# Performance work log

Measured on AMD Instinct MI355X. Metric: run time of the kernel, lower is better.

## Reference

```python
import jax, jax.numpy as jnp
import numpy as np

N_NODES = 100000
N_EDGES = 1600000
D_IN = 128
D_HID = 128


def setup_inputs() -> dict:
    key = jax.random.key(0)
    ks = jax.random.split(key, 7)
    s_in = 1.0 / np.sqrt(D_IN)
    s_hid = 1.0 / np.sqrt(D_HID)
    return {
        "x": jax.random.normal(ks[0], (N_NODES, D_IN), dtype=jnp.float32),
        "edge_index": jax.random.randint(ks[1], (2, N_EDGES), 0, N_NODES, dtype=jnp.int64),
        "W1_l": jax.random.normal(ks[2], (D_IN, D_HID), dtype=jnp.float32) * s_in,
        "b1": jnp.zeros((D_HID,), dtype=jnp.float32),
        "W1_r": jax.random.normal(ks[3], (D_IN, D_HID), dtype=jnp.float32) * s_in,
        "W2_l": jax.random.normal(ks[4], (D_HID, D_HID), dtype=jnp.float32) * s_hid,
        "b2": jnp.zeros((D_HID,), dtype=jnp.float32),
        "W2_r": jax.random.normal(ks[5], (D_HID, D_HID), dtype=jnp.float32) * s_hid,
    }


def _mean_aggregate(x, src, dst, num_nodes):
    # messages x[src] mean-aggregated at dst (PyG SAGEConv default aggr='mean')
    msg = jnp.take(x, src, axis=0)                       # [E, D] gather
    summed = jax.ops.segment_sum(msg, dst, num_segments=num_nodes)  # [N, D]
    deg = jax.ops.segment_sum(jnp.ones((src.shape[0],), x.dtype), dst,
                              num_segments=num_nodes)
    return summed / jnp.maximum(deg, 1.0)[:, None]


def _sage_conv(x, src, dst, W_l, b, W_r):
    agg = _mean_aggregate(x, src, dst, x.shape[0])
    # out = lin_l(aggregated neighbors) + lin_r(root)
    return agg @ W_l + b + x @ W_r


def reference(x, edge_index, W1_l, b1, W1_r, W2_l, b2, W2_r):
    src, dst = edge_index[0], edge_index[1]
    h = _sage_conv(x, src, dst, W1_l, b1, W1_r)
    h = jax.nn.relu(h)  # dropout inactive in eval mode
    out = _sage_conv(h, src, dst, W2_l, b2, W2_r)
    return out
```

## Files before the change

### kernel.cpp

```cpp
#include <hip/hip_runtime.h>

#define NN 100000
#define NE 1600000
#define DF 128
#define NBUCK 391
#define PA_BLOCKS 784
#define PB_BLOCKS 391
#define CX_BLOCKS 3125
#define CW_BLOCKS 64
#define AGG_GRID 3128

typedef short short8 __attribute__((ext_vector_type(8)));
typedef float floatx4 __attribute__((ext_vector_type(4)));
typedef float floatx2 __attribute__((ext_vector_type(2)));
typedef unsigned int uintx4 __attribute__((ext_vector_type(4)));
typedef unsigned int uint;
typedef unsigned short ushort;
typedef unsigned char uchar;

static __device__ __forceinline__ ushort f2bf(float f) {
    uint u = __builtin_bit_cast(uint, f);
    return (ushort)((u + 0x7fffu + ((u >> 16) & 1u)) >> 16);
}

__global__ __launch_bounds__(256) void pA_hist(const int* __restrict__ dst,
                                               int* __restrict__ gcnt) {
    __shared__ int h[NBUCK];
    int tid = threadIdx.x;
    for (int i = tid; i < NBUCK; i += 256) h[i] = 0;
    __syncthreads();
    int eb = blockIdx.x * 2048 + tid;
    #pragma unroll
    for (int k = 0; k < 8; ++k) {
        int e = eb + k * 256;
        if (e < NE) atomicAdd(&h[dst[e] >> 8], 1);
    }
    __syncthreads();
    for (int i = tid; i < NBUCK; i += 256)
        if (h[i]) atomicAdd(&gcnt[i], h[i]);
}

__global__ __launch_bounds__(512) void pS_scan(const int* __restrict__ gcnt,
                                               int* __restrict__ goff,
                                               int* __restrict__ gcur) {
    __shared__ int s[512];
    int tid = threadIdx.x;
    int v = (tid < NBUCK) ? gcnt[tid] : 0;
    s[tid] = v;
    __syncthreads();
    for (int st = 1; st < 512; st <<= 1) {
        int t = (tid >= st) ? s[tid - st] : 0;
        __syncthreads();
        s[tid] += t;
        __syncthreads();
    }
    if (tid < NBUCK) {
        int e = s[tid] - v;
        goff[tid] = e;
        gcur[tid] = e;
    }
    if (tid == 0) goff[NBUCK] = NE;
}

__global__ __launch_bounds__(512) void fused_mid(
        const int* __restrict__ src, const int* __restrict__ dst,
        int* __restrict__ gcur, uint2* __restrict__ pairs,
        const float* __restrict__ x, ushort* __restrict__ xb, uint* __restrict__ xf8,
        const float* __restrict__ W1l, const float* __restrict__ W1r,
        const float* __restrict__ W2l, const float* __restrict__ W2r,
        ushort* __restrict__ WT1, ushort* __restrict__ WT2) {
    __shared__ int h[NBUCK];
    __shared__ int base[NBUCK];
    int bid = blockIdx.x;
    int tid = threadIdx.x;
    if (bid < PB_BLOCKS) {
        for (int i = tid; i < NBUCK; i += 512) h[i] = 0;
        __syncthreads();
        int eb = bid * 4096 + tid;
        int bkt[8], dv[8];
        #pragma unroll
        for (int k = 0; k < 8; ++k) {
            int e = eb + k * 512;
            bkt[k] = -1;
            if (e < NE) {
                int d = dst[e];
                dv[k] = d;
                bkt[k] = d >> 8;
                atomicAdd(&h[bkt[k]], 1);
            }
        }
        __syncthreads();
        for (int i = tid; i < NBUCK; i += 512) {
            base[i] = h[i] ? atomicAdd(&gcur[i], h[i]) : 0;
            h[i] = 0;
        }
        __syncthreads();
        #pragma unroll
        for (int k = 0; k < 8; ++k) {
            int e = eb + k * 512;
            if (e < NE) {
                int r = atomicAdd(&h[bkt[k]], 1);
                pairs[base[bkt[k]] + r] = make_uint2((uint)src[e], (uint)dv[k]);
            }
        }
    } else if (bid < PB_BLOCKS + CX_BLOCKS) {
        int j = (bid - PB_BLOCKS) * 512 + tid;
        const float4* xr = (const float4*)x + (size_t)j * 2;
        float4 v0 = xr[0], v1 = xr[1];
        uint4 ob;
        ob.x = (uint)f2bf(v0.x) | ((uint)f2bf(v0.y) << 16);
        ob.y = (uint)f2bf(v0.z) | ((uint)f2bf(v0.w) << 16);
        ob.z = (uint)f2bf(v1.x) | ((uint)f2bf(v1.y) << 16);
        ob.w = (uint)f2bf(v1.z) | ((uint)f2bf(v1.w) << 16);
        ((uint4*)xb)[j] = ob;
        uint pk0 = (uint)__builtin_amdgcn_cvt_pk_fp8_f32(v0.x, v0.y, 0, false);
        pk0 = (uint)__builtin_amdgcn_cvt_pk_fp8_f32(v0.z, v0.w, (int)pk0, true);
        uint pk1 = (uint)__builtin_amdgcn_cvt_pk_fp8_f32(v1.x, v1.y, 0, false);
        pk1 = (uint)__builtin_amdgcn_cvt_pk_fp8_f32(v1.z, v1.w, (int)pk1, true);
        ((uint2*)xf8)[j] = make_uint2(pk0, pk1);
    } else {
        int id = (bid - PB_BLOCKS - CX_BLOCKS) * 512 + tid;
        int n = id >> 8, k = id & 255;
        float a = (k < 128) ? W1l[k * 128 + n] : W1r[(k - 128) * 128 + n];
        float b = (k < 128) ? W2l[k * 128 + n] : W2r[(k - 128) * 128 + n];
        WT1[id] = f2bf(a);
        WT2[id] = f2bf(b);
    }
}

__global__ __launch_bounds__(256) void pC_scatter(const uint2* __restrict__ pairs,
                                                  const int* __restrict__ goff,
                                                  int* __restrict__ off,
                                                  int* __restrict__ srt) {
    __shared__ int deg[256];
    __shared__ int loc[256];
    int b = blockIdx.x;
    int beg = goff[b], end = goff[b + 1];
    int tid = threadIdx.x;
    deg[tid] = 0;
    __syncthreads();
    for (int i = beg + tid; i < end; i += 256)
        atomicAdd(&deg[pairs[i].y & 255], 1);
    __syncthreads();
    int v = deg[tid];
    loc[tid] = v;
    __syncthreads();
    for (int st = 1; st < 256; st <<= 1) {
        int t = (tid >= st) ? loc[tid - st] : 0;
        __syncthreads();
        loc[tid] += t;
        __syncthreads();
    }
    int excl = loc[tid] - v + beg;
    int n = (b << 8) + tid;
    if (n < NN) off[n] = excl;
    __syncthreads();
    deg[tid] = excl;
    __syncthreads();
    for (int i = beg + tid; i < end; i += 256) {
        uint2 pr = pairs[i];
        int pos = atomicAdd(&deg[pr.y & 255], 1);
        srt[pos] = (int)pr.x;
    }
}

static __device__ __forceinline__ void acc16(floatx2* ac, uint4 v) {
    ac[0] += __builtin_amdgcn_cvt_pk_f32_fp8((int)v.x, false);
    ac[1] += __builtin_amdgcn_cvt_pk_f32_fp8((int)v.x, true);
    ac[2] += __builtin_amdgcn_cvt_pk_f32_fp8((int)v.y, false);
    ac[3] += __builtin_amdgcn_cvt_pk_f32_fp8((int)v.y, true);
    ac[4] += __builtin_amdgcn_cvt_pk_f32_fp8((int)v.z, false);
    ac[5] += __builtin_amdgcn_cvt_pk_f32_fp8((int)v.z, true);
    ac[6] += __builtin_amdgcn_cvt_pk_f32_fp8((int)v.w, false);
    ac[7] += __builtin_amdgcn_cvt_pk_f32_fp8((int)v.w, true);
}

#define AGG_LOOP(IDX)                                            \
    {                                                            \
        int i = lb;                                              \
        for (; i + 8 <= le; i += 8) {                            \
            int idx[8];                                          \
            _Pragma("unroll")                                    \
            for (int k = 0; k < 8; ++k) idx[k] = IDX(i + k);     \
            uint4 v[8];                                          \
            _Pragma("unroll")                                    \
            for (int k = 0; k < 8; ++k) v[k] = f[(size_t)idx[k] * 8]; \
            _Pragma("unroll")                                    \
            for (int k = 0; k < 8; ++k) acc16(ac, v[k]);         \
        }                                                        \
        if (i + 4 <= le) {                                       \
            int idx[4];                                          \
            _Pragma("unroll")                                    \
            for (int k = 0; k < 4; ++k) idx[k] = IDX(i + k);     \
            uint4 v[4];                                          \
            _Pragma("unroll")                                    \
            for (int k = 0; k < 4; ++k) v[k] = f[(size_t)idx[k] * 8]; \
            _Pragma("unroll")                                    \
            for (int k = 0; k < 4; ++k) acc16(ac, v[k]);         \
            i += 4;                                              \
        }                                                        \
        for (; i < le; ++i) {                                    \
            uint4 v = f[(size_t)IDX(i) * 8];                     \
            acc16(ac, v);                                        \
        }                                                        \
    }

__global__ __launch_bounds__(256) void agg_csr(const uint* __restrict__ feat8,
                                               const int* __restrict__ srt,
                                               const int* __restrict__ off,
                                               ushort* __restrict__ aggb) {
    __shared__ int sidx[2048];
    int nb = blockIdx.x * 32;
    if (nb >= NN) return;
    int tid = threadIdx.x;

    int segb = off[nb];
    int nend = nb + 32;
    int sege = (nend < NN) ? off[nend] : NE;
    int stage = min(sege - segb, 2048);
    for (int i = tid; i < stage; i += 256) sidx[i] = srt[segb + i];
    __syncthreads();

    int n = nb + (tid >> 3);
    int l = tid & 7;
    if (n >= NN) return;
    const uint4* f = (const uint4*)feat8 + l;

    int beg = off[n];
    int end = (n < NN - 1) ? off[n + 1] : NE;
    int lb = beg - segb, le = end - segb;

    floatx2 ac[8];
    #pragma unroll
    for (int t = 0; t < 8; ++t) ac[t] = (floatx2){0.f, 0.f};

    if (le <= stage) {
        #define IDX_LDS(ii) sidx[ii]
        AGG_LOOP(IDX_LDS)
        #undef IDX_LDS
    } else {
        #define IDX_GBL(ii) srt[segb + (ii)]
        AGG_LOOP(IDX_GBL)
        #undef IDX_GBL
    }

    float inv = 1.0f / fmaxf((float)(end - beg), 1.0f);
    uintx4 o0, o1;
    o0.x = (uint)f2bf(ac[0].x * inv) | ((uint)f2bf(ac[0].y * inv) << 16);
    o0.y = (uint)f2bf(ac[1].x * inv) | ((uint)f2bf(ac[1].y * inv) << 16);
    o0.z = (uint)f2bf(ac[2].x * inv) | ((uint)f2bf(ac[2].y * inv) << 16);
    o0.w = (uint)f2bf(ac[3].x * inv) | ((uint)f2bf(ac[3].y * inv) << 16);
    o1.x = (uint)f2bf(ac[4].x * inv) | ((uint)f2bf(ac[4].y * inv) << 16);
    o1.y = (uint)f2bf(ac[5].x * inv) | ((uint)f2bf(ac[5].y * inv) << 16);
    o1.z = (uint)f2bf(ac[6].x * inv) | ((uint)f2bf(ac[6].y * inv) << 16);
    o1.w = (uint)f2bf(ac[7].x * inv) | ((uint)f2bf(ac[7].y * inv) << 16);
    uintx4* dp = (uintx4*)(aggb + (size_t)n * 128 + l * 16);
    __builtin_nontemporal_store(o0, dp);
    __builtin_nontemporal_store(o1, dp + 1);
}

template <int RELU, int BF16OUT, int F8OUT>
__global__ __launch_bounds__(512, 4) void gemm_mfma(
        const ushort* __restrict__ aggb, const ushort* __restrict__ selfb,
        const ushort* __restrict__ WT, const float* __restrict__ bias,
        void* __restrict__ outv, uchar* __restrict__ f8out) {
    __shared__ ushort sWT[128 * 256];
    const int tid = threadIdx.x;
    const int blk = blockIdx.x;

    #pragma unroll
    for (int it = 0; it < 8; ++it) {
        int flat = it * 512 + tid;
        int col = flat >> 5;
        int c = flat & 31;
        uint4 v = *(const uint4*)(WT + (size_t)col * 256 + c * 8);
        *(uint4*)&sWT[col * 256 + (c ^ (col & 7)) * 8] = v;
    }

    const int w = tid >> 6;
    const int lane = tid & 63;
    const int m = lane & 15;
    const int q = lane >> 4;

    int node_m = blk * 128 + w * 16 + m;
    int cn = node_m < NN ? node_m : NN - 1;
    const ushort* arow = aggb + (size_t)cn * 128;
    const ushort* xrow = selfb + (size_t)cn * 128;
    short8 a[8];
    #pragma unroll
    for (int kk = 0; kk < 4; ++kk) {
        a[kk]     = *(const short8*)(arow + kk * 32 + q * 8);
        a[4 + kk] = *(const short8*)(xrow + kk * 32 + q * 8);
    }

    __syncthreads();

    floatx4 acc[8];
    #pragma unroll
    for (int t = 0; t < 8; ++t) acc[t] = (floatx4){0.f, 0.f, 0.f, 0.f};

    const int m7 = m & 7;
    #pragma unroll
    for (int kk = 0; kk < 8; ++kk) {
        int cx = (kk * 4 + q) ^ m7;
        #pragma unroll
        for (int t = 0; t < 8; ++t) {
            short8 b = *(const short8*)&sWT[(t * 16 + m) * 256 + cx * 8];
            acc[t] = __builtin_amdgcn_mfma_f32_16x16x32_bf16(a[kk], b, acc[t], 0, 0, 0);
        }
    }

    const int node_base = blk * 128 + w * 16 + q * 4;
    #pragma unroll
    for (int t = 0; t < 8; ++t) {
        int col = t * 16 + m;
        float bj = bias[col];
        #pragma unroll
        for (int r = 0; r < 4; ++r) {
            int node = node_base + r;
            if (node < NN) {
                float v = acc[t][r] + bj;
                if (RELU) v = fmaxf(v, 0.0f);
                if (BF16OUT)
                    ((ushort*)outv)[(size_t)node * 128 + col] = f2bf(v);
                else
                    ((float*)outv)[(size_t)node * 128 + col] = v;
                if (F8OUT) {
                    uint pk = (uint)__builtin_amdgcn_cvt_pk_fp8_f32(v, v, 0, false);
                    f8out[(size_t)node * 128 + col] = (uchar)pk;
                }
            }
        }
    }
}

extern "C" void kernel_launch(void* const* d_in, const int* in_sizes, int n_in,
                              void* d_out, int out_size, void* d_ws, size_t ws_size,
                              hipStream_t stream) {
    const float* x   = (const float*)d_in[0];
    const int*   ei  = (const int*)d_in[1];
    const float* W1l = (const float*)d_in[2];
    const float* b1  = (const float*)d_in[3];
    const float* W1r = (const float*)d_in[4];
    const float* W2l = (const float*)d_in[5];
    const float* b2  = (const float*)d_in[6];
    const float* W2r = (const float*)d_in[7];
    float*       out = (float*)d_out;

    const int* src = ei;
    const int* dst = ei + NE;

    char* ws = (char*)d_ws;
    int*    off  = (int*)(ws);
    int*    srt  = (int*)(ws + 400000);
    ushort* WT1  = (ushort*)(ws + 7200000);
    ushort* WT2  = (ushort*)(ws + 7265536);
    ushort* xb   = (ushort*)(ws + 7331072);
    uint*   xf8  = (uint*)(ws + 32931072);
    ushort* aggb = (ushort*)(ws + 45731072);
    ushort* hb   = (ushort*)(ws + 71331072);
    uchar*  hf8  = (uchar*)xf8;
    uint2*  pairs = (uint2*)aggb;
    int*    gcnt  = (int*)((char*)aggb + 12800000);
    int*    goff  = (int*)((char*)aggb + 12801600);
    int*    gcur  = (int*)((char*)aggb + 12803200);

    (void)hipMemsetAsync(gcnt, 0, NBUCK * 4, stream);
    pA_hist<<<PA_BLOCKS, 256, 0, stream>>>(dst, gcnt);
    pS_scan<<<1, 512, 0, stream>>>(gcnt, goff, gcur);
    fused_mid<<<PB_BLOCKS + CX_BLOCKS + CW_BLOCKS, 512, 0, stream>>>(
        src, dst, gcur, pairs, x, xb, xf8, W1l, W1r, W2l, W2r, WT1, WT2);
    pC_scatter<<<NBUCK, 256, 0, stream>>>(pairs, goff, off, srt);

    const int gemm_grid = (NN + 127) / 128;

    agg_csr<<<AGG_GRID, 256, 0, stream>>>(xf8, srt, off, aggb);
    gemm_mfma<1, 1, 1><<<gemm_grid, 512, 0, stream>>>(aggb, xb, WT1, b1, hb, hf8);

    agg_csr<<<AGG_GRID, 256, 0, stream>>>((const uint*)hf8, srt, off, aggb);
    gemm_mfma<0, 0, 0><<<gemm_grid, 512, 0, stream>>>(aggb, hb, WT2, b2, out, nullptr);
}
```

Before: 195.2 us.

## Replace atomic bucket partitioning with per-block histogram, column scan, and stored ranks

The histogram pass now records each edge's local rank within its block bucket and writes per-block histograms instead of atomically accumulating global counts. A new column-scan kernel computes per-block exclusive offsets for each bucket, so the partition pass can compute each edge's destination deterministically without shared-memory atomics or global atomicAdd on cursors. This removes the memset, the duplicated histogram and atomics in fused_mid, at the cost of an extra kernel launch and extra traffic for the 3.2MB rank array and 1.2MB histogram table.

```diff
diff --git a/kernel.cpp b/kernel.cpp
--- a/kernel.cpp
+++ b/kernel.cpp
@@ -24,7 +24,8 @@
 }
 
 __global__ __launch_bounds__(256) void pA_hist(const int* __restrict__ dst,
-                                               int* __restrict__ gcnt) {
+                                               int* __restrict__ hist,
+                                               ushort* __restrict__ rank8) {
     __shared__ int h[NBUCK];
     int tid = threadIdx.x;
     for (int i = tid; i < NBUCK; i += 256) h[i] = 0;
@@ -33,19 +34,52 @@
     #pragma unroll
     for (int k = 0; k < 8; ++k) {
         int e = eb + k * 256;
-        if (e < NE) atomicAdd(&h[dst[e] >> 8], 1);
-    }
-    __syncthreads();
-    for (int i = tid; i < NBUCK; i += 256)
-        if (h[i]) atomicAdd(&gcnt[i], h[i]);
-}
-
-__global__ __launch_bounds__(512) void pS_scan(const int* __restrict__ gcnt,
-                                               int* __restrict__ goff,
-                                               int* __restrict__ gcur) {
+        if (e < NE) {
+            int r = atomicAdd(&h[dst[e] >> 8], 1);
+            rank8[e] = (ushort)r;
+        }
+    }
+    __syncthreads();
+    int* hrow = hist + blockIdx.x * NBUCK;
+    for (int i = tid; i < NBUCK; i += 256) hrow[i] = h[i];
+}
+
+__global__ __launch_bounds__(256) void pS2_colscan(int* __restrict__ hist,
+                                                   int* __restrict__ gt) {
+    __shared__ int ps[256];
+    int b = blockIdx.x;
+    int tid = threadIdx.x;
+    int v[4];
+    int sum = 0;
+    #pragma unroll
+    for (int k = 0; k < 4; ++k) {
+        int blk = tid * 4 + k;
+        v[k] = (blk < PA_BLOCKS) ? hist[blk * NBUCK + b] : 0;
+        sum += v[k];
+    }
+    ps[tid] = sum;
+    __syncthreads();
+    for (int st = 1; st < 256; st <<= 1) {
+        int t = (tid >= st) ? ps[tid - st] : 0;
+        __syncthreads();
+        ps[tid] += t;
+        __syncthreads();
+    }
+    int excl = ps[tid] - sum;
+    #pragma unroll
+    for (int k = 0; k < 4; ++k) {
+        int blk = tid * 4 + k;
+        if (blk < PA_BLOCKS) hist[blk * NBUCK + b] = excl;
+        excl += v[k];
+    }
+    if (tid == 255) gt[b] = excl;
+}
+
+__global__ __launch_bounds__(512) void pS_scan(const int* __restrict__ gt,
+                                               int* __restrict__ goff) {
     __shared__ int s[512];
     int tid = threadIdx.x;
-    int v = (tid < NBUCK) ? gcnt[tid] : 0;
+    int v = (tid < NBUCK) ? gt[tid] : 0;
     s[tid] = v;
     __syncthreads();
     for (int st = 1; st < 512; st <<= 1) {
@@ -54,53 +88,31 @@
         s[tid] += t;
         __syncthreads();
     }
-    if (tid < NBUCK) {
-        int e = s[tid] - v;
-        goff[tid] = e;
-        gcur[tid] = e;
-    }
+    if (tid < NBUCK) goff[tid] = s[tid] - v;
     if (tid == 0) goff[NBUCK] = NE;
 }
 
 __global__ __launch_bounds__(512) void fused_mid(
         const int* __restrict__ src, const int* __restrict__ dst,
-        int* __restrict__ gcur, uint2* __restrict__ pairs,
+        const ushort* __restrict__ rank8, const int* __restrict__ rel,
+        const int* __restrict__ goff, uint2* __restrict__ pairs,
         const float* __restrict__ x, ushort* __restrict__ xb, uint* __restrict__ xf8,
         const float* __restrict__ W1l, const float* __restrict__ W1r,
         const float* __restrict__ W2l, const float* __restrict__ W2r,
         ushort* __restrict__ WT1, ushort* __restrict__ WT2) {
-    __shared__ int h[NBUCK];
-    __shared__ int base[NBUCK];
     int bid = blockIdx.x;
     int tid = threadIdx.x;
     if (bid < PB_BLOCKS) {
-        for (int i = tid; i < NBUCK; i += 512) h[i] = 0;
-        __syncthreads();
         int eb = bid * 4096 + tid;
-        int bkt[8], dv[8];
-        #pragma unroll
-        for (int k = 0; k < 8; ++k) {
-            int e = eb + k * 512;
-            bkt[k] = -1;
-            if (e < NE) {
-                int d = dst[e];
-                dv[k] = d;
-                bkt[k] = d >> 8;
-                atomicAdd(&h[bkt[k]], 1);
-            }
-        }
-        __syncthreads();
-        for (int i = tid; i < NBUCK; i += 512) {
-            base[i] = h[i] ? atomicAdd(&gcur[i], h[i]) : 0;
-            h[i] = 0;
-        }
-        __syncthreads();
         #pragma unroll
         for (int k = 0; k < 8; ++k) {
             int e = eb + k * 512;
             if (e < NE) {
-                int r = atomicAdd(&h[bkt[k]], 1);
-                pairs[base[bkt[k]] + r] = make_uint2((uint)src[e], (uint)dv[k]);
+                int s = src[e];
+                int d = dst[e];
+                int b = d >> 8;
+                int pos = goff[b] + rel[(e >> 11) * NBUCK + b] + (int)rank8[e];
+                pairs[pos] = make_uint2((uint)s, (uint)d);
             }
         }
     } else if (bid < PB_BLOCKS + CX_BLOCKS) {
@@ -361,15 +373,17 @@
     ushort* hb   = (ushort*)(ws + 71331072);
     uchar*  hf8  = (uchar*)xf8;
     uint2*  pairs = (uint2*)aggb;
-    int*    gcnt  = (int*)((char*)aggb + 12800000);
-    int*    goff  = (int*)((char*)aggb + 12801600);
-    int*    gcur  = (int*)((char*)aggb + 12803200);
-
-    (void)hipMemsetAsync(gcnt, 0, NBUCK * 4, stream);
-    pA_hist<<<PA_BLOCKS, 256, 0, stream>>>(dst, gcnt);
-    pS_scan<<<1, 512, 0, stream>>>(gcnt, goff, gcur);
+    int*    hist  = (int*)((char*)aggb + 12800000);
+    ushort* rank8 = (ushort*)((char*)aggb + 14100000);
+    int*    gt    = (int*)((char*)aggb + 17300000);
+    int*    goff  = (int*)((char*)aggb + 17302000);
+
+    pA_hist<<<PA_BLOCKS, 256, 0, stream>>>(dst, hist, rank8);
+    pS2_colscan<<<NBUCK, 256, 0, stream>>>(hist, gt);
+    pS_scan<<<1, 512, 0, stream>>>(gt, goff);
     fused_mid<<<PB_BLOCKS + CX_BLOCKS + CW_BLOCKS, 512, 0, stream>>>(
-        src, dst, gcur, pairs, x, xb, xf8, W1l, W1r, W2l, W2r, WT1, WT2);
+        src, dst, rank8, hist, goff, pairs, x, xb, xf8,
+        W1l, W1r, W2l, W2r, WT1, WT2);
     pC_scatter<<<NBUCK, 256, 0, stream>>>(pairs, goff, off, srt);
 
     const int gemm_grid = (NN + 127) / 128;
```

After: 183.7 us. 1.06x faster.
